# Performance work log

Measured on AMD Instinct MI355X. Metric: run time of the kernel, lower is better.

The kernel has to match this reference:

```python
import jax, jax.numpy as jnp
import numpy as np

B, T, D_Q, D_K, D_W = 128, 4096, 16, 16, 32


def setup_inputs() -> dict:
    key0 = jax.random.key(0)
    ks = jax.random.split(key0, 8)
    return {
        "query": jax.random.normal(ks[0], (B, 1, D_Q), dtype=jnp.float32),
        "key": jax.random.normal(ks[1], (B, T, D_K), dtype=jnp.float32),
        "value": jax.random.normal(ks[2], (B, T, D_K), dtype=jnp.float32),
        "W1": jax.random.normal(ks[3], (D_W, D_Q), dtype=jnp.float32) * 0.1,
        "W2": jax.random.normal(ks[4], (D_W, D_K), dtype=jnp.float32) * 0.1,
        "bias": jax.random.uniform(ks[5], (), dtype=jnp.float32, minval=-0.1, maxval=0.1),
        "v_w": jax.random.normal(ks[6], (1, D_W), dtype=jnp.float32) * 0.1,
        "v_b": jax.random.normal(ks[7], (1,), dtype=jnp.float32) * 0.1,
    }


def reference(query, key, value, W1, W2, bias, v_w, v_b):
    # Bahdanau additive attention.
    # query: [B,1,d_q], key/value: [B,T,d_k]
    q_proj = jnp.einsum('bqd,wd->bqw', query, W1)      # [B,1,d_w]
    k_proj = jnp.einsum('btd,wd->btw', key, W2)        # [B,T,d_w]
    h = jnp.tanh(k_proj + q_proj + bias)               # [B,T,d_w]
    score = (jnp.einsum('btw,ow->bto', h, v_w) + v_b).squeeze(-1)  # [B,T]
    attn = jax.nn.softmax(score, axis=-1)              # [B,T]
    context = jnp.einsum('bt,btd->bd', attn, value)[:, None, :]    # [B,1,d_v]
    return context, attn
```

## Files before the change

### kernel.cpp

```cpp
#include <hip/hip_runtime.h>

#define NB 128
#define NT 4096
#define DKD 16
#define DW 32
#define CHUNKS 4
#define TC 1024
#define BLK 256
#define PT 4

__device__ __forceinline__ float fast_tanh(float x) {
    float e = __expf(2.0f * x);
    return 1.0f - 2.0f * __builtin_amdgcn_rcpf(e + 1.0f);
}

__global__ __launch_bounds__(BLK) void aa_score(
    const float* __restrict__ query, const float* __restrict__ key,
    const float* __restrict__ value, const float* __restrict__ W1,
    const float* __restrict__ W2, const float* __restrict__ bias,
    const float* __restrict__ v_w, const float* __restrict__ v_b,
    float* __restrict__ attn,
    float* __restrict__ ws_l,
    float* __restrict__ ws_ctx)
{
    const int b   = blockIdx.x / CHUNKS;
    const int c   = blockIdx.x % CHUNKS;
    const int tid = threadIdx.x;

    __shared__ float s_w2[DW * DKD];
    __shared__ float s_comb[DW];
    __shared__ float s_vw[DW];
    __shared__ float s_rctx[4 * 16];
    __shared__ float s_rl[4];

    if (tid < 128)
        reinterpret_cast<float4*>(s_w2)[tid] = reinterpret_cast<const float4*>(W2)[tid];
    if (tid >= 128 && tid < 128 + DW) {
        const int w = tid - 128;
        float acc = bias[0];
        const float* q  = query + b * DKD;
        const float* w1 = W1 + w * DKD;
        #pragma unroll
        for (int d = 0; d < DKD; ++d) acc = fmaf(q[d], w1[d], acc);
        s_comb[w] = acc;
        s_vw[w]   = v_w[w];
    }
    __syncthreads();

    const float vb = v_b[0];
    const size_t tbase = (size_t)b * NT + (size_t)c * TC + (size_t)tid * PT;
    const float4* kp = reinterpret_cast<const float4*>(key)   + tbase * 4;
    const float4* vp = reinterpret_cast<const float4*>(value) + tbase * 4;

    float4 k0[PT], k1[PT], k2[PT], k3[PT];
    #pragma unroll
    for (int j = 0; j < PT; ++j) {
        k0[j] = kp[4*j + 0]; k1[j] = kp[4*j + 1];
        k2[j] = kp[4*j + 2]; k3[j] = kp[4*j + 3];
    }

    float sc[PT];
    #pragma unroll
    for (int j = 0; j < PT; ++j) sc[j] = vb;

    #pragma unroll 4
    for (int w = 0; w < DW; ++w) {
        const float4* wr = reinterpret_cast<const float4*>(s_w2 + w * DKD);
        const float4 w0 = wr[0], w1 = wr[1], w2 = wr[2], w3 = wr[3];
        const float cw = s_comb[w];
        const float vw = s_vw[w];
        #pragma unroll
        for (int j = 0; j < PT; ++j) {
            float h = cw;
            h = fmaf(k0[j].x, w0.x, h); h = fmaf(k0[j].y, w0.y, h);
            h = fmaf(k0[j].z, w0.z, h); h = fmaf(k0[j].w, w0.w, h);
            h = fmaf(k1[j].x, w1.x, h); h = fmaf(k1[j].y, w1.y, h);
            h = fmaf(k1[j].z, w1.z, h); h = fmaf(k1[j].w, w1.w, h);
            h = fmaf(k2[j].x, w2.x, h); h = fmaf(k2[j].y, w2.y, h);
            h = fmaf(k2[j].z, w2.z, h); h = fmaf(k2[j].w, w2.w, h);
            h = fmaf(k3[j].x, w3.x, h); h = fmaf(k3[j].y, w3.y, h);
            h = fmaf(k3[j].z, w3.z, h); h = fmaf(k3[j].w, w3.w, h);
            sc[j] = fmaf(fast_tanh(h), vw, sc[j]);
        }
    }

    float l = 0.0f;
    float ctx[16];
    #pragma unroll
    for (int d = 0; d < 16; ++d) ctx[d] = 0.0f;

    float p[PT];
    #pragma unroll
    for (int j = 0; j < PT; ++j) {
        p[j] = __expf(sc[j]);
        l += p[j];
        const float4 v0 = vp[4*j + 0], v1 = vp[4*j + 1];
        const float4 v2 = vp[4*j + 2], v3 = vp[4*j + 3];
        ctx[ 0] = fmaf(p[j], v0.x, ctx[ 0]); ctx[ 1] = fmaf(p[j], v0.y, ctx[ 1]);
        ctx[ 2] = fmaf(p[j], v0.z, ctx[ 2]); ctx[ 3] = fmaf(p[j], v0.w, ctx[ 3]);
        ctx[ 4] = fmaf(p[j], v1.x, ctx[ 4]); ctx[ 5] = fmaf(p[j], v1.y, ctx[ 5]);
        ctx[ 6] = fmaf(p[j], v1.z, ctx[ 6]); ctx[ 7] = fmaf(p[j], v1.w, ctx[ 7]);
        ctx[ 8] = fmaf(p[j], v2.x, ctx[ 8]); ctx[ 9] = fmaf(p[j], v2.y, ctx[ 9]);
        ctx[10] = fmaf(p[j], v2.z, ctx[10]); ctx[11] = fmaf(p[j], v2.w, ctx[11]);
        ctx[12] = fmaf(p[j], v3.x, ctx[12]); ctx[13] = fmaf(p[j], v3.y, ctx[13]);
        ctx[14] = fmaf(p[j], v3.z, ctx[14]); ctx[15] = fmaf(p[j], v3.w, ctx[15]);
    }
    reinterpret_cast<float4*>(attn + (size_t)b * NT + (size_t)c * TC)[tid] =
        make_float4(p[0], p[1], p[2], p[3]);

    #pragma unroll
    for (int o = 32; o > 0; o >>= 1) l += __shfl_xor(l, o);
    #pragma unroll
    for (int d = 0; d < 16; ++d) {
        #pragma unroll
        for (int o = 32; o > 0; o >>= 1) ctx[d] += __shfl_xor(ctx[d], o);
    }
    const int wave = tid >> 6;
    const int lane = tid & 63;
    if (lane == 0) {
        s_rl[wave] = l;
        #pragma unroll
        for (int d = 0; d < 16; ++d) s_rctx[wave * 16 + d] = ctx[d];
    }
    __syncthreads();
    const int slot = b * CHUNKS + c;
    if (tid < 16)
        ws_ctx[slot * 16 + tid] =
            s_rctx[tid] + s_rctx[16 + tid] + s_rctx[32 + tid] + s_rctx[48 + tid];
    if (tid == 0)
        ws_l[slot] = s_rl[0] + s_rl[1] + s_rl[2] + s_rl[3];
}

__global__ __launch_bounds__(BLK) void aa_finish(
    float* __restrict__ out,
    const float* __restrict__ ws_l,
    const float* __restrict__ ws_ctx)
{
    const int b   = blockIdx.x / CHUNKS;
    const int c   = blockIdx.x % CHUNKS;
    const int tid = threadIdx.x;
    const float L = ws_l[b*CHUNKS + 0] + ws_l[b*CHUNKS + 1] +
                    ws_l[b*CHUNKS + 2] + ws_l[b*CHUNKS + 3];
    const float inv = 1.0f / L;

    float4* ap = reinterpret_cast<float4*>(out + NB*DKD + (size_t)b * NT + (size_t)c * TC);
    float4 p = ap[tid];
    p.x *= inv; p.y *= inv; p.z *= inv; p.w *= inv;
    ap[tid] = p;

    if (c == 0 && tid < DKD) {
        const float* wc = ws_ctx + b * CHUNKS * 16;
        out[b * DKD + tid] = (wc[tid] + wc[16 + tid] + wc[32 + tid] + wc[48 + tid]) * inv;
    }
}

extern "C" void kernel_launch(void* const* d_in, const int* in_sizes, int n_in,
                              void* d_out, int out_size, void* d_ws, size_t ws_size,
                              hipStream_t stream) {
    const float* query = (const float*)d_in[0];
    const float* key   = (const float*)d_in[1];
    const float* value = (const float*)d_in[2];
    const float* W1    = (const float*)d_in[3];
    const float* W2    = (const float*)d_in[4];
    const float* bias  = (const float*)d_in[5];
    const float* v_w   = (const float*)d_in[6];
    const float* v_b   = (const float*)d_in[7];
    float* out = (float*)d_out;

    float* ws_l   = (float*)d_ws;
    float* ws_ctx = ws_l + NB * CHUNKS;

    aa_score<<<NB * CHUNKS, BLK, 0, stream>>>(
        query, key, value, W1, W2, bias, v_w, v_b,
        out + NB * DKD, ws_l, ws_ctx);
    aa_finish<<<NB * CHUNKS, BLK, 0, stream>>>(out, ws_l, ws_ctx);
}
```

Measured before the change: 119.0 us.

## Fuse score and normalize kernels with per-batch atomic counter spin barrier

Merges the two kernels into one. Blocks of the same batch row signal completion through an atomic counter and spin until all chunks arrive, then write the normalized attention and context directly. This drops the second launch and the attn read-modify-write round trip. It also doubles the chunk count with fewer tokens per thread and prefetches value alongside key. The spin barrier assumes all 1024 blocks can be co-resident, or at least that every batch's chunks get scheduled, and it adds a memset launch.

```diff
diff --git a/kernel.cpp b/kernel.cpp
--- a/kernel.cpp
+++ b/kernel.cpp
@@ -4,27 +4,28 @@
 #define NT 4096
 #define DKD 16
 #define DW 32
-#define CHUNKS 4
-#define TC 1024
+#define CHUNKS 8
+#define TC 512
 #define BLK 256
-#define PT 4
+#define PT 2
 
 __device__ __forceinline__ float fast_tanh(float x) {
     float e = __expf(2.0f * x);
     return 1.0f - 2.0f * __builtin_amdgcn_rcpf(e + 1.0f);
 }
 
-__global__ __launch_bounds__(BLK) void aa_score(
+__global__ __launch_bounds__(BLK, 4) void aa_fused(
     const float* __restrict__ query, const float* __restrict__ key,
     const float* __restrict__ value, const float* __restrict__ W1,
     const float* __restrict__ W2, const float* __restrict__ bias,
     const float* __restrict__ v_w, const float* __restrict__ v_b,
-    float* __restrict__ attn,
+    float* __restrict__ out,
     float* __restrict__ ws_l,
-    float* __restrict__ ws_ctx)
+    float* __restrict__ ws_ctx,
+    unsigned int* __restrict__ ws_cnt)
 {
-    const int b   = blockIdx.x / CHUNKS;
-    const int c   = blockIdx.x % CHUNKS;
+    const int b   = blockIdx.x >> 3;
+    const int c   = blockIdx.x & (CHUNKS - 1);
     const int tid = threadIdx.x;
 
     __shared__ float s_w2[DW * DKD];
@@ -32,6 +33,7 @@
     __shared__ float s_vw[DW];
     __shared__ float s_rctx[4 * 16];
     __shared__ float s_rl[4];
+    __shared__ float s_inv;
 
     if (tid < 128)
         reinterpret_cast<float4*>(s_w2)[tid] = reinterpret_cast<const float4*>(W2)[tid];
@@ -53,10 +55,16 @@
     const float4* vp = reinterpret_cast<const float4*>(value) + tbase * 4;
 
     float4 k0[PT], k1[PT], k2[PT], k3[PT];
+    float4 v0[PT], v1[PT], v2[PT], v3[PT];
     #pragma unroll
     for (int j = 0; j < PT; ++j) {
         k0[j] = kp[4*j + 0]; k1[j] = kp[4*j + 1];
         k2[j] = kp[4*j + 2]; k3[j] = kp[4*j + 3];
+    }
+    #pragma unroll
+    for (int j = 0; j < PT; ++j) {
+        v0[j] = vp[4*j + 0]; v1[j] = vp[4*j + 1];
+        v2[j] = vp[4*j + 2]; v3[j] = vp[4*j + 3];
     }
 
     float sc[PT];
@@ -94,19 +102,15 @@
     for (int j = 0; j < PT; ++j) {
         p[j] = __expf(sc[j]);
         l += p[j];
-        const float4 v0 = vp[4*j + 0], v1 = vp[4*j + 1];
-        const float4 v2 = vp[4*j + 2], v3 = vp[4*j + 3];
-        ctx[ 0] = fmaf(p[j], v0.x, ctx[ 0]); ctx[ 1] = fmaf(p[j], v0.y, ctx[ 1]);
-        ctx[ 2] = fmaf(p[j], v0.z, ctx[ 2]); ctx[ 3] = fmaf(p[j], v0.w, ctx[ 3]);
-        ctx[ 4] = fmaf(p[j], v1.x, ctx[ 4]); ctx[ 5] = fmaf(p[j], v1.y, ctx[ 5]);
-        ctx[ 6] = fmaf(p[j], v1.z, ctx[ 6]); ctx[ 7] = fmaf(p[j], v1.w, ctx[ 7]);
-        ctx[ 8] = fmaf(p[j], v2.x, ctx[ 8]); ctx[ 9] = fmaf(p[j], v2.y, ctx[ 9]);
-        ctx[10] = fmaf(p[j], v2.z, ctx[10]); ctx[11] = fmaf(p[j], v2.w, ctx[11]);
-        ctx[12] = fmaf(p[j], v3.x, ctx[12]); ctx[13] = fmaf(p[j], v3.y, ctx[13]);
-        ctx[14] = fmaf(p[j], v3.z, ctx[14]); ctx[15] = fmaf(p[j], v3.w, ctx[15]);
+        ctx[ 0] = fmaf(p[j], v0[j].x, ctx[ 0]); ctx[ 1] = fmaf(p[j], v0[j].y, ctx[ 1]);
+        ctx[ 2] = fmaf(p[j], v0[j].z, ctx[ 2]); ctx[ 3] = fmaf(p[j], v0[j].w, ctx[ 3]);
+        ctx[ 4] = fmaf(p[j], v1[j].x, ctx[ 4]); ctx[ 5] = fmaf(p[j], v1[j].y, ctx[ 5]);
+        ctx[ 6] = fmaf(p[j], v1[j].z, ctx[ 6]); ctx[ 7] = fmaf(p[j], v1[j].w, ctx[ 7]);
+        ctx[ 8] = fmaf(p[j], v2[j].x, ctx[ 8]); ctx[ 9] = fmaf(p[j], v2[j].y, ctx[ 9]);
+        ctx[10] = fmaf(p[j], v2[j].z, ctx[10]); ctx[11] = fmaf(p[j], v2[j].w, ctx[11]);
+        ctx[12] = fmaf(p[j], v3[j].x, ctx[12]); ctx[13] = fmaf(p[j], v3[j].y, ctx[13]);
+        ctx[14] = fmaf(p[j], v3[j].z, ctx[14]); ctx[15] = fmaf(p[j], v3[j].w, ctx[15]);
     }
-    reinterpret_cast<float4*>(attn + (size_t)b * NT + (size_t)c * TC)[tid] =
-        make_float4(p[0], p[1], p[2], p[3]);
 
     #pragma unroll
     for (int o = 32; o > 0; o >>= 1) l += __shfl_xor(l, o);
@@ -123,34 +127,44 @@
         for (int d = 0; d < 16; ++d) s_rctx[wave * 16 + d] = ctx[d];
     }
     __syncthreads();
+
     const int slot = b * CHUNKS + c;
     if (tid < 16)
-        ws_ctx[slot * 16 + tid] =
-            s_rctx[tid] + s_rctx[16 + tid] + s_rctx[32 + tid] + s_rctx[48 + tid];
+        __hip_atomic_store(&ws_ctx[slot * 16 + tid],
+            s_rctx[tid] + s_rctx[16 + tid] + s_rctx[32 + tid] + s_rctx[48 + tid],
+            __ATOMIC_RELAXED, __HIP_MEMORY_SCOPE_AGENT);
     if (tid == 0)
-        ws_l[slot] = s_rl[0] + s_rl[1] + s_rl[2] + s_rl[3];
-}
+        __hip_atomic_store(&ws_l[slot], s_rl[0] + s_rl[1] + s_rl[2] + s_rl[3],
+            __ATOMIC_RELAXED, __HIP_MEMORY_SCOPE_AGENT);
+    __syncthreads();
 
-__global__ __launch_bounds__(BLK) void aa_finish(
-    float* __restrict__ out,
-    const float* __restrict__ ws_l,
-    const float* __restrict__ ws_ctx)
-{
-    const int b   = blockIdx.x / CHUNKS;
-    const int c   = blockIdx.x % CHUNKS;
-    const int tid = threadIdx.x;
-    const float L = ws_l[b*CHUNKS + 0] + ws_l[b*CHUNKS + 1] +
-                    ws_l[b*CHUNKS + 2] + ws_l[b*CHUNKS + 3];
-    const float inv = 1.0f / L;
+    if (tid == 0) {
+        __threadfence();
+        atomicAdd(&ws_cnt[b], 1u);
+        while (__hip_atomic_load(&ws_cnt[b], __ATOMIC_RELAXED,
+                                 __HIP_MEMORY_SCOPE_AGENT) < CHUNKS)
+            __builtin_amdgcn_s_sleep(2);
+        __threadfence();
+        float L = 0.0f;
+        #pragma unroll
+        for (int i = 0; i < CHUNKS; ++i)
+            L += __hip_atomic_load(&ws_l[b * CHUNKS + i], __ATOMIC_RELAXED,
+                                   __HIP_MEMORY_SCOPE_AGENT);
+        s_inv = 1.0f / L;
+    }
+    __syncthreads();
+    const float inv = s_inv;
 
-    float4* ap = reinterpret_cast<float4*>(out + NB*DKD + (size_t)b * NT + (size_t)c * TC);
-    float4 p = ap[tid];
-    p.x *= inv; p.y *= inv; p.z *= inv; p.w *= inv;
-    ap[tid] = p;
+    reinterpret_cast<float2*>(out + NB * DKD + (size_t)b * NT + (size_t)c * TC)[tid] =
+        make_float2(p[0] * inv, p[1] * inv);
 
     if (c == 0 && tid < DKD) {
-        const float* wc = ws_ctx + b * CHUNKS * 16;
-        out[b * DKD + tid] = (wc[tid] + wc[16 + tid] + wc[32 + tid] + wc[48 + tid]) * inv;
+        float s = 0.0f;
+        #pragma unroll
+        for (int i = 0; i < CHUNKS; ++i)
+            s += __hip_atomic_load(&ws_ctx[(b * CHUNKS + i) * 16 + tid],
+                                   __ATOMIC_RELAXED, __HIP_MEMORY_SCOPE_AGENT);
+        out[b * DKD + tid] = s * inv;
     }
 }
 
@@ -167,11 +181,13 @@
     const float* v_b   = (const float*)d_in[7];
     float* out = (float*)d_out;
 
-    float* ws_l   = (float*)d_ws;
+    unsigned int* ws_cnt = (unsigned int*)d_ws;
+    float* ws_l   = (float*)d_ws + NB;
     float* ws_ctx = ws_l + NB * CHUNKS;
 
-    aa_score<<<NB * CHUNKS, BLK, 0, stream>>>(
+    hipMemsetAsync(d_ws, 0, NB * sizeof(unsigned int), stream);
+
+    aa_fused<<<NB * CHUNKS, BLK, 0, stream>>>(
         query, key, value, W1, W2, bias, v_w, v_b,
-        out + NB * DKD, ws_l, ws_ctx);
-    aa_finish<<<NB * CHUNKS, BLK, 0, stream>>>(out, ws_l, ws_ctx);
+        out, ws_l, ws_ctx, ws_cnt);
 }
```

Result: slower. 173.9 us (+46.1%).

## Fuse score and finish kernels into one 1024-thread block per batch

Applied to the files above, without the earlier changes.

Replaces the two-kernel split (chunked score pass writing unnormalized attn plus a finish pass rescaling it) with a single kernel in which one 1024-thread block covers a whole batch row. The block-wide reduction of the softmax sum and context happens in shared memory, so normalized attention is written once and the read-modify-write of attn in a second launch goes away. It also packs comb and v_w into an interleaved float2. The cost is only 128 blocks for the whole GPU, which may leave compute units underused on a large device.

```diff
diff --git a/kernel.cpp b/kernel.cpp
--- a/kernel.cpp
+++ b/kernel.cpp
@@ -4,9 +4,7 @@
 #define NT 4096
 #define DKD 16
 #define DW 32
-#define CHUNKS 4
-#define TC 1024
-#define BLK 256
+#define BLK 1024
 #define PT 4
 
 __device__ __forceinline__ float fast_tanh(float x) {
@@ -14,24 +12,20 @@
     return 1.0f - 2.0f * __builtin_amdgcn_rcpf(e + 1.0f);
 }
 
-__global__ __launch_bounds__(BLK) void aa_score(
+__global__ __launch_bounds__(BLK, 1) void aa_fused(
     const float* __restrict__ query, const float* __restrict__ key,
     const float* __restrict__ value, const float* __restrict__ W1,
     const float* __restrict__ W2, const float* __restrict__ bias,
     const float* __restrict__ v_w, const float* __restrict__ v_b,
-    float* __restrict__ attn,
-    float* __restrict__ ws_l,
-    float* __restrict__ ws_ctx)
+    float* __restrict__ out)
 {
-    const int b   = blockIdx.x / CHUNKS;
-    const int c   = blockIdx.x % CHUNKS;
+    const int b   = blockIdx.x;
     const int tid = threadIdx.x;
 
     __shared__ float s_w2[DW * DKD];
-    __shared__ float s_comb[DW];
-    __shared__ float s_vw[DW];
-    __shared__ float s_rctx[4 * 16];
-    __shared__ float s_rl[4];
+    __shared__ float s_cv[DW * 2];
+    __shared__ float s_red[16 * 17];
+    __shared__ float s_fin[17];
 
     if (tid < 128)
         reinterpret_cast<float4*>(s_w2)[tid] = reinterpret_cast<const float4*>(W2)[tid];
@@ -42,13 +36,13 @@
         const float* w1 = W1 + w * DKD;
         #pragma unroll
         for (int d = 0; d < DKD; ++d) acc = fmaf(q[d], w1[d], acc);
-        s_comb[w] = acc;
-        s_vw[w]   = v_w[w];
+        s_cv[2 * w]     = acc;
+        s_cv[2 * w + 1] = v_w[w];
     }
     __syncthreads();
 
     const float vb = v_b[0];
-    const size_t tbase = (size_t)b * NT + (size_t)c * TC + (size_t)tid * PT;
+    const size_t tbase = (size_t)b * NT + (size_t)tid * PT;
     const float4* kp = reinterpret_cast<const float4*>(key)   + tbase * 4;
     const float4* vp = reinterpret_cast<const float4*>(value) + tbase * 4;
 
@@ -67,11 +61,10 @@
     for (int w = 0; w < DW; ++w) {
         const float4* wr = reinterpret_cast<const float4*>(s_w2 + w * DKD);
         const float4 w0 = wr[0], w1 = wr[1], w2 = wr[2], w3 = wr[3];
-        const float cw = s_comb[w];
-        const float vw = s_vw[w];
+        const float2 cv = *reinterpret_cast<const float2*>(s_cv + 2 * w);
         #pragma unroll
         for (int j = 0; j < PT; ++j) {
-            float h = cw;
+            float h = cv.x;
             h = fmaf(k0[j].x, w0.x, h); h = fmaf(k0[j].y, w0.y, h);
             h = fmaf(k0[j].z, w0.z, h); h = fmaf(k0[j].w, w0.w, h);
             h = fmaf(k1[j].x, w1.x, h); h = fmaf(k1[j].y, w1.y, h);
@@ -80,7 +73,7 @@
             h = fmaf(k2[j].z, w2.z, h); h = fmaf(k2[j].w, w2.w, h);
             h = fmaf(k3[j].x, w3.x, h); h = fmaf(k3[j].y, w3.y, h);
             h = fmaf(k3[j].z, w3.z, h); h = fmaf(k3[j].w, w3.w, h);
-            sc[j] = fmaf(fast_tanh(h), vw, sc[j]);
+            sc[j] = fmaf(fast_tanh(h), cv.y, sc[j]);
         }
     }
 
@@ -105,8 +98,6 @@
         ctx[12] = fmaf(p[j], v3.x, ctx[12]); ctx[13] = fmaf(p[j], v3.y, ctx[13]);
         ctx[14] = fmaf(p[j], v3.z, ctx[14]); ctx[15] = fmaf(p[j], v3.w, ctx[15]);
     }
-    reinterpret_cast<float4*>(attn + (size_t)b * NT + (size_t)c * TC)[tid] =
-        make_float4(p[0], p[1], p[2], p[3]);
 
     #pragma unroll
     for (int o = 32; o > 0; o >>= 1) l += __shfl_xor(l, o);
@@ -118,40 +109,26 @@
     const int wave = tid >> 6;
     const int lane = tid & 63;
     if (lane == 0) {
-        s_rl[wave] = l;
         #pragma unroll
-        for (int d = 0; d < 16; ++d) s_rctx[wave * 16 + d] = ctx[d];
+        for (int d = 0; d < 16; ++d) s_red[wave * 17 + d] = ctx[d];
+        s_red[wave * 17 + 16] = l;
     }
     __syncthreads();
-    const int slot = b * CHUNKS + c;
-    if (tid < 16)
-        ws_ctx[slot * 16 + tid] =
-            s_rctx[tid] + s_rctx[16 + tid] + s_rctx[32 + tid] + s_rctx[48 + tid];
-    if (tid == 0)
-        ws_l[slot] = s_rl[0] + s_rl[1] + s_rl[2] + s_rl[3];
-}
+    if (tid < 17) {
+        float s = 0.0f;
+        #pragma unroll
+        for (int wv = 0; wv < 16; ++wv) s += s_red[wv * 17 + tid];
+        s_fin[tid] = s;
+    }
+    __syncthreads();
 
-__global__ __launch_bounds__(BLK) void aa_finish(
-    float* __restrict__ out,
-    const float* __restrict__ ws_l,
-    const float* __restrict__ ws_ctx)
-{
-    const int b   = blockIdx.x / CHUNKS;
-    const int c   = blockIdx.x % CHUNKS;
-    const int tid = threadIdx.x;
-    const float L = ws_l[b*CHUNKS + 0] + ws_l[b*CHUNKS + 1] +
-                    ws_l[b*CHUNKS + 2] + ws_l[b*CHUNKS + 3];
-    const float inv = 1.0f / L;
+    const float inv = 1.0f / s_fin[16];
 
-    float4* ap = reinterpret_cast<float4*>(out + NB*DKD + (size_t)b * NT + (size_t)c * TC);
-    float4 p = ap[tid];
-    p.x *= inv; p.y *= inv; p.z *= inv; p.w *= inv;
-    ap[tid] = p;
+    reinterpret_cast<float4*>(out + NB * DKD + (size_t)b * NT)[tid] =
+        make_float4(p[0] * inv, p[1] * inv, p[2] * inv, p[3] * inv);
 
-    if (c == 0 && tid < DKD) {
-        const float* wc = ws_ctx + b * CHUNKS * 16;
-        out[b * DKD + tid] = (wc[tid] + wc[16 + tid] + wc[32 + tid] + wc[48 + tid]) * inv;
-    }
+    if (tid < DKD)
+        out[b * DKD + tid] = s_fin[tid] * inv;
 }
 
 extern "C" void kernel_launch(void* const* d_in, const int* in_sizes, int n_in,
@@ -167,11 +144,6 @@
     const float* v_b   = (const float*)d_in[7];
     float* out = (float*)d_out;
 
-    float* ws_l   = (float*)d_ws;
-    float* ws_ctx = ws_l + NB * CHUNKS;
-
-    aa_score<<<NB * CHUNKS, BLK, 0, stream>>>(
-        query, key, value, W1, W2, bias, v_w, v_b,
-        out + NB * DKD, ws_l, ws_ctx);
-    aa_finish<<<NB * CHUNKS, BLK, 0, stream>>>(out, ws_l, ws_ctx);
+    aa_fused<<<NB, BLK, 0, stream>>>(
+        query, key, value, W1, W2, bias, v_w, v_b, out);
 }
```

Result: slower. 140.7 us (+18.2%).
